# Kernel optimization log

Measured on AMD Instinct MI355X. Metric: run time of the kernel, lower is better.

Reference implementation:

```python
import jax, jax.numpy as jnp
import numpy as np

B, S, E, H = 2, 2048, 1024, 16
D = E // H  # head_dim = 64


def setup_inputs() -> dict:
    key = jax.random.key(0)
    k1, k2, k3 = jax.random.split(key, 3)
    scale_in = 1.0 / np.sqrt(E)
    return {
        "x": jax.random.normal(k1, (B, S, E), dtype=jnp.float32),
        "W_attn": jax.random.normal(k2, (E, 3 * E), dtype=jnp.float32) * scale_in,
        "b_attn": jnp.zeros((3 * E,), dtype=jnp.float32),
        "W_proj": jax.random.normal(k3, (E, E), dtype=jnp.float32) * scale_in,
        "b_proj": jnp.zeros((E,), dtype=jnp.float32),
    }


def reference(x, W_attn, b_attn, W_proj, b_proj):
    # c_attn: fused QKV projection  [B,S,E] -> [B,S,3E]
    qkv = x @ W_attn + b_attn
    q, k, v = jnp.split(qkv, 3, axis=-1)
    # split heads -> [B,S,H,D]
    q = q.reshape(B, S, H, D)
    k = k.reshape(B, S, H, D)
    v = v.reshape(B, S, H, D)
    # scaled dot-product attention (no causal mask in the source module)
    scores = jnp.einsum("bqhd,bkhd->bhqk", q, k) / jnp.sqrt(jnp.float32(D))
    attn = jax.nn.softmax(scores, axis=-1)  # attn_dropout is identity in eval
    y = jnp.einsum("bhqk,bkhd->bqhd", attn, v).reshape(B, S, E)
    # c_proj; resid_dropout is identity in eval
    return y @ W_proj + b_proj
```

## Files before the change

### kernel.cpp

```cpp
#include <hip/hip_runtime.h>
#include <stdint.h>

#define NB 2
#define NS 2048
#define NE 1024
#define NH 16
#define ND 64
#define NE3 3072
#define NBS 4096

typedef _Float16 half8 __attribute__((ext_vector_type(8)));
typedef __fp16 fp16x2 __attribute__((ext_vector_type(2)));
typedef float f32x4 __attribute__((ext_vector_type(4)));
typedef float f32x16 __attribute__((ext_vector_type(16)));
typedef unsigned int u32;

__device__ __forceinline__ void gload16(const void* g, void* l) {
  __builtin_amdgcn_global_load_lds(
      (__attribute__((address_space(1))) void*)const_cast<void*>(g),
      (__attribute__((address_space(3))) void*)l, 16, 0, 0);
}

__global__ void k_cvt16(const float* __restrict__ src, _Float16* __restrict__ dst, int n8) {
  int i = blockIdx.x * blockDim.x + threadIdx.x;
  if (i >= n8) return;
  const float4* s = (const float4*)src + (size_t)i * 2;
  float4 a = s[0], b = s[1];
  half8 o;
  o[0]=(_Float16)a.x; o[1]=(_Float16)a.y; o[2]=(_Float16)a.z; o[3]=(_Float16)a.w;
  o[4]=(_Float16)b.x; o[5]=(_Float16)b.y; o[6]=(_Float16)b.z; o[7]=(_Float16)b.w;
  *((half8*)dst + i) = o;
}

__global__ void k_cvtT(const float* __restrict__ src, _Float16* __restrict__ dst, int K, int N) {
  __shared__ _Float16 tile[64][72];
  int n0 = blockIdx.x * 64, k0 = blockIdx.y * 64;
  int t = threadIdx.x;
  int kk = t >> 2, nc = (t & 3) << 4;
  const float* sp = src + (size_t)(k0 + kk) * N + n0 + nc;
#pragma unroll
  for (int j = 0; j < 16; j += 4) {
    float4 v = *(const float4*)(sp + j);
    tile[kk][nc + j + 0] = (_Float16)v.x;
    tile[kk][nc + j + 1] = (_Float16)v.y;
    tile[kk][nc + j + 2] = (_Float16)v.z;
    tile[kk][nc + j + 3] = (_Float16)v.w;
  }
  __syncthreads();
  int nn = t >> 2, kc = (t & 3) << 4;
  half8 o0, o1;
#pragma unroll
  for (int j = 0; j < 8; ++j) { o0[j] = tile[kc + j][nn]; o1[j] = tile[kc + 8 + j][nn]; }
  _Float16* op = dst + (size_t)(n0 + nn) * K + k0 + kc;
  *(half8*)op = o0;
  *(half8*)(op + 8) = o1;
}

template <int OUT_HALF>
__global__ __launch_bounds__(256, 2)
void k_gemm(const _Float16* __restrict__ A, const _Float16* __restrict__ Bt,
            const float* __restrict__ bias, void* __restrict__ Cv,
            int M, int N, int K) {
  __shared__ _Float16 As[128 * 32];
  __shared__ _Float16 Bs[128 * 32];
  const int nwg = gridDim.x * gridDim.y;
  const int d = blockIdx.y * gridDim.x + blockIdx.x;
  const int lid = (d & 7) * (nwg >> 3) + (d >> 3);
  const int bx = lid % gridDim.x, by = lid / gridDim.x;
  const int m0 = by * 128, n0 = bx * 128;
  const int t = threadIdx.x, l = t & 63, w = t >> 6;
  const int wr = w >> 1, wc = w & 1;
  const int srow = l >> 2;
  const int sk = (l & 3) << 3;
  f32x4 acc[4][4] = {};
  for (int kt = 0; kt < K; kt += 32) {
    __syncthreads();
#pragma unroll
    for (int i = 0; i < 2; ++i) {
      int rb = (i * 4 + w) * 16;
      gload16(A + (size_t)(m0 + rb + srow) * K + kt + sk, (char*)As + (i * 4 + w) * 1024);
      gload16(Bt + (size_t)(n0 + rb + srow) * K + kt + sk, (char*)Bs + (i * 4 + w) * 1024);
    }
    __syncthreads();
    half8 a[4], b[4];
#pragma unroll
    for (int i = 0; i < 4; ++i)
      a[i] = *(const half8*)(As + (wr * 64 + i * 16 + (l & 15)) * 32 + ((l >> 4) << 3));
#pragma unroll
    for (int j = 0; j < 4; ++j)
      b[j] = *(const half8*)(Bs + (wc * 64 + j * 16 + (l & 15)) * 32 + ((l >> 4) << 3));
#pragma unroll
    for (int i = 0; i < 4; ++i)
#pragma unroll
      for (int j = 0; j < 4; ++j)
        acc[i][j] = __builtin_amdgcn_mfma_f32_16x16x32_f16(a[i], b[j], acc[i][j], 0, 0, 0);
  }
  float bv[4];
#pragma unroll
  for (int j = 0; j < 4; ++j) bv[j] = bias[n0 + wc * 64 + j * 16 + (l & 15)];
#pragma unroll
  for (int i = 0; i < 4; ++i) {
    int row0 = m0 + wr * 64 + i * 16 + ((l >> 4) << 2);
#pragma unroll
    for (int j = 0; j < 4; ++j) {
      int col = n0 + wc * 64 + j * 16 + (l & 15);
#pragma unroll
      for (int r = 0; r < 4; ++r) {
        float v = acc[i][j][r] + bv[j];
        if (OUT_HALF)
          ((_Float16*)Cv)[(size_t)(row0 + r) * N + col] = (_Float16)v;
        else
          ((float*)Cv)[(size_t)(row0 + r) * N + col] = v;
      }
    }
  }
}

__global__ void k_vt(const _Float16* __restrict__ qkv, _Float16* __restrict__ Vt) {
  __shared__ _Float16 tile[64][72];
  int s0 = blockIdx.x * 64;
  int bh = blockIdx.y, b = bh >> 4, h = bh & 15;
  int t = threadIdx.x;
  int ss = t >> 2, dc = (t & 3) << 4;
  const _Float16* sp = qkv + (size_t)(b * NS + s0 + ss) * NE3 + 2 * NE + h * ND + dc;
  half8 v0 = *(const half8*)sp, v1 = *(const half8*)(sp + 8);
#pragma unroll
  for (int j = 0; j < 8; ++j) { tile[ss][dc + j] = v0[j]; tile[ss][dc + 8 + j] = v1[j]; }
  __syncthreads();
  int d = t >> 2, sc = (t & 3) << 4;
  half8 o0, o1;
#pragma unroll
  for (int j = 0; j < 8; ++j) { o0[j] = tile[sc + j][d]; o1[j] = tile[sc + 8 + j][d]; }
  _Float16* op = Vt + (size_t)(bh * ND + d) * NS + s0 + sc;
  *(half8*)op = o0;
  *(half8*)(op + 8) = o1;
}

__global__ __launch_bounds__(256, 2)
void k_attn(const _Float16* __restrict__ qkv, const _Float16* __restrict__ Vt,
            _Float16* __restrict__ Y) {
  __shared__ _Float16 Kb[2][64 * 64];
  __shared__ _Float16 Vb[2][64 * 64];
  const int dly = blockIdx.y * gridDim.x + blockIdx.x;
  const int lid = (dly & 7) * 64 + (dly >> 3);
  const int bh = lid >> 4, qb = lid & 15;
  const int q0 = qb * 128;
  const int b = bh >> 4, h = bh & 15;
  const int t = threadIdx.x, l = t & 63, w = t >> 6;
  const int c = l & 31, hh = l >> 5;
  const float cexp = 0.125f * 1.44269504088896340736f;

  half8 qf[4];
  {
    const _Float16* qp = qkv + (size_t)(b * NS + q0 + w * 32 + c) * NE3 + h * ND + 8 * hh;
    qf[0] = *(const half8*)(qp);
    qf[1] = *(const half8*)(qp + 16);
    qf[2] = *(const half8*)(qp + 32);
    qf[3] = *(const half8*)(qp + 48);
  }

  f32x16 Oa0 = {}, Oa1 = {}, Osum = {};
  half8 ones;
#pragma unroll
  for (int j = 0; j < 8; ++j) ones[j] = (_Float16)1.0f;

  const int row8 = l >> 3;
  const int d0s_base = (l & 7) << 3;

#define STAGE_KV(KT, BUF)                                                            \
  {                                                                                  \
    _Pragma("unroll")                                                                \
    for (int i = 0; i < 2; ++i) {                                                    \
      int ci = w * 2 + i;                                                            \
      int row = ci * 8 + row8;                                                       \
      int d0s = d0s_base ^ ((row & 7) << 3);                                         \
      gload16(qkv + (size_t)(b * NS + (KT) * 64 + row) * NE3 + NE + h * ND + d0s,    \
              (char*)&Kb[BUF][0] + ci * 1024);                                       \
      gload16(Vt + (size_t)(bh * ND + row) * NS + (KT) * 64 + d0s,                   \
              (char*)&Vb[BUF][0] + ci * 1024);                                       \
    }                                                                                \
  }

  STAGE_KV(0, 0);
  __syncthreads();

  for (int kt = 0; kt < NS / 64; ++kt) {
    const int cur = kt & 1;
    if (kt + 1 < NS / 64) STAGE_KV(kt + 1, cur ^ 1);

    f32x16 sa0 = {}, sa1 = {};
#pragma unroll
    for (int tt = 0; tt < 4; ++tt) {
      int chs = ((2 * tt + hh) ^ (c & 7)) << 4;
      half8 kf0 = *(const half8*)((char*)&Kb[cur][0] + c * 128 + chs);
      half8 kf1 = *(const half8*)((char*)&Kb[cur][0] + (32 + c) * 128 + chs);
      sa0 = __builtin_amdgcn_mfma_f32_32x32x16_f16(kf0, qf[tt], sa0, 0, 0, 0);
      sa1 = __builtin_amdgcn_mfma_f32_32x32x16_f16(kf1, qf[tt], sa1, 0, 0, 0);
    }

    u32 D0[4][2], D1[4][2];
#pragma unroll
    for (int s = 0; s < 4; ++s) {
      fp16x2 e0 = __builtin_amdgcn_cvt_pkrtz(__builtin_amdgcn_exp2f(sa0[4 * s + 0] * cexp),
                                             __builtin_amdgcn_exp2f(sa0[4 * s + 1] * cexp));
      fp16x2 e1 = __builtin_amdgcn_cvt_pkrtz(__builtin_amdgcn_exp2f(sa0[4 * s + 2] * cexp),
                                             __builtin_amdgcn_exp2f(sa0[4 * s + 3] * cexp));
      fp16x2 e2 = __builtin_amdgcn_cvt_pkrtz(__builtin_amdgcn_exp2f(sa1[4 * s + 0] * cexp),
                                             __builtin_amdgcn_exp2f(sa1[4 * s + 1] * cexp));
      fp16x2 e3 = __builtin_amdgcn_cvt_pkrtz(__builtin_amdgcn_exp2f(sa1[4 * s + 2] * cexp),
                                             __builtin_amdgcn_exp2f(sa1[4 * s + 3] * cexp));
      D0[s][0] = __builtin_bit_cast(u32, e0);
      D0[s][1] = __builtin_bit_cast(u32, e1);
      D1[s][0] = __builtin_bit_cast(u32, e2);
      D1[s][1] = __builtin_bit_cast(u32, e3);
    }

#define PVSTEP(KK, DARR)                                                              \
    {                                                                                 \
      u32 pb0 = DARR[2 * ((KK) & 1)][0], pa0 = DARR[2 * ((KK) & 1) + 1][0];           \
      u32 pb1 = DARR[2 * ((KK) & 1)][1], pa1 = DARR[2 * ((KK) & 1) + 1][1];           \
      u32 sent0 = hh ? pb0 : pa0;                                                     \
      u32 sent1 = hh ? pb1 : pa1;                                                     \
      u32 recv0 = __shfl_xor(sent0, 32);                                              \
      u32 recv1 = __shfl_xor(sent1, 32);                                              \
      union { u32 d[4]; half8 h; } pfu;                                               \
      pfu.d[0] = hh ? recv0 : pb0;                                                    \
      pfu.d[1] = hh ? recv1 : pb1;                                                    \
      pfu.d[2] = hh ? pa0 : recv0;                                                    \
      pfu.d[3] = hh ? pa1 : recv1;                                                    \
      int chv = ((2 * (KK) + hh) ^ (c & 7)) << 4;                                     \
      half8 vf0 = *(const half8*)((char*)&Vb[cur][0] + c * 128 + chv);                \
      half8 vf1 = *(const half8*)((char*)&Vb[cur][0] + (32 + c) * 128 + chv);         \
      Oa0 = __builtin_amdgcn_mfma_f32_32x32x16_f16(pfu.h, vf0, Oa0, 0, 0, 0);         \
      Oa1 = __builtin_amdgcn_mfma_f32_32x32x16_f16(pfu.h, vf1, Oa1, 0, 0, 0);         \
      Osum = __builtin_amdgcn_mfma_f32_32x32x16_f16(pfu.h, ones, Osum, 0, 0, 0);      \
    }
    PVSTEP(0, D0)
    PVSTEP(1, D0)
    PVSTEP(2, D1)
    PVSTEP(3, D1)
#undef PVSTEP

    __syncthreads();
  }

#pragma unroll
  for (int i = 0; i < 16; ++i) {
    int ql = (i & 3) + 8 * (i >> 2) + 4 * hh;
    float inv = 1.0f / Osum[i];
    size_t base = (size_t)(b * NS + q0 + w * 32 + ql) * NE + h * ND + c;
    Y[base] = (_Float16)(Oa0[i] * inv);
    Y[base + 32] = (_Float16)(Oa1[i] * inv);
  }
}

extern "C" void kernel_launch(void* const* d_in, const int* in_sizes, int n_in,
                              void* d_out, int out_size, void* d_ws, size_t ws_size,
                              hipStream_t stream) {
  (void)in_sizes; (void)n_in; (void)out_size; (void)ws_size;
  const float* x      = (const float*)d_in[0];
  const float* W_attn = (const float*)d_in[1];
  const float* b_attn = (const float*)d_in[2];
  const float* W_proj = (const float*)d_in[3];
  const float* b_proj = (const float*)d_in[4];
  char* ws = (char*)d_ws;
  const size_t MB = 1024 * 1024;
  _Float16* qkvb = (_Float16*)(ws);
  _Float16* WaT  = (_Float16*)(ws + 24 * MB);
  _Float16* WpT  = (_Float16*)(ws + 30 * MB);
  _Float16* xb   = (_Float16*)(ws + 32 * MB);
  _Float16* Vt   = (_Float16*)(ws + 40 * MB);
  _Float16* yb   = (_Float16*)(ws + 32 * MB);

  k_cvt16<<<dim3(2048), dim3(256), 0, stream>>>(x, xb, NBS * NE / 8);
  k_cvtT<<<dim3(48, 16), dim3(256), 0, stream>>>(W_attn, WaT, NE, NE3);
  k_cvtT<<<dim3(16, 16), dim3(256), 0, stream>>>(W_proj, WpT, NE, NE);
  k_gemm<1><<<dim3(NE3 / 128, NBS / 128), dim3(256), 0, stream>>>(xb, WaT, b_attn, (void*)qkvb, NBS, NE3, NE);
  k_vt<<<dim3(NS / 64, NB * NH), dim3(256), 0, stream>>>(qkvb, Vt);
  k_attn<<<dim3(NS / 128, NB * NH), dim3(256), 0, stream>>>(qkvb, Vt, yb);
  k_gemm<0><<<dim3(NE / 128, NBS / 128), dim3(256), 0, stream>>>(yb, WpT, b_proj, d_out, NBS, NE, NE);
}
```

Before: 135.6 us.

## Software-pipeline QK of next tile with PV and fold softmax scale into Q

The attention loop is restructured so the QK^T MFMAs for the next key tile are issued between the exp stage and the PV MFMAs of the current tile. K and V staging are split and staggered so K runs one tile further ahead than V. The loop is unrolled by two with ping-pong score registers. Separately, the softmax scale times log2(e) is folded into the Q columns in the QKV GEMM epilogue, which removes a multiply per score element. The cost is higher register pressure, a more complex buffer-reuse schedule, and Q rounded to fp16 after scaling.

```diff
diff --git a/kernel.cpp b/kernel.cpp
--- a/kernel.cpp
+++ b/kernel.cpp
@@ -8,6 +8,7 @@
 #define ND 64
 #define NE3 3072
 #define NBS 4096
+#define NT 32
 
 typedef _Float16 half8 __attribute__((ext_vector_type(8)));
 typedef __fp16 fp16x2 __attribute__((ext_vector_type(2)));
@@ -107,6 +108,7 @@
 #pragma unroll
       for (int r = 0; r < 4; ++r) {
         float v = acc[i][j][r] + bv[j];
+        if (OUT_HALF && col < NE) v *= 0.18033688011112042f;
         if (OUT_HALF)
           ((_Float16*)Cv)[(size_t)(row0 + r) * N + col] = (_Float16)v;
         else
@@ -148,7 +150,6 @@
   const int b = bh >> 4, h = bh & 15;
   const int t = threadIdx.x, l = t & 63, w = t >> 6;
   const int c = l & 31, hh = l >> 5;
-  const float cexp = 0.125f * 1.44269504088896340736f;
 
   half8 qf[4];
   {
@@ -160,6 +161,7 @@
   }
 
   f32x16 Oa0 = {}, Oa1 = {}, Osum = {};
+  f32x16 saE0, saE1, saO0, saO1;
   half8 ones;
 #pragma unroll
   for (int j = 0; j < 8; ++j) ones[j] = (_Float16)1.0f;
@@ -167,7 +169,7 @@
   const int row8 = l >> 3;
   const int d0s_base = (l & 7) << 3;
 
-#define STAGE_KV(KT, BUF)                                                            \
+#define STAGE_K(KT, BUF)                                                             \
   {                                                                                  \
     _Pragma("unroll")                                                                \
     for (int i = 0; i < 2; ++i) {                                                    \
@@ -176,46 +178,34 @@
       int d0s = d0s_base ^ ((row & 7) << 3);                                         \
       gload16(qkv + (size_t)(b * NS + (KT) * 64 + row) * NE3 + NE + h * ND + d0s,    \
               (char*)&Kb[BUF][0] + ci * 1024);                                       \
+    }                                                                                \
+  }
+#define STAGE_V(KT, BUF)                                                             \
+  {                                                                                  \
+    _Pragma("unroll")                                                                \
+    for (int i = 0; i < 2; ++i) {                                                    \
+      int ci = w * 2 + i;                                                            \
+      int row = ci * 8 + row8;                                                       \
+      int d0s = d0s_base ^ ((row & 7) << 3);                                         \
       gload16(Vt + (size_t)(bh * ND + row) * NS + (KT) * 64 + d0s,                   \
               (char*)&Vb[BUF][0] + ci * 1024);                                       \
     }                                                                                \
   }
 
-  STAGE_KV(0, 0);
-  __syncthreads();
-
-  for (int kt = 0; kt < NS / 64; ++kt) {
-    const int cur = kt & 1;
-    if (kt + 1 < NS / 64) STAGE_KV(kt + 1, cur ^ 1);
-
-    f32x16 sa0 = {}, sa1 = {};
-#pragma unroll
-    for (int tt = 0; tt < 4; ++tt) {
-      int chs = ((2 * tt + hh) ^ (c & 7)) << 4;
-      half8 kf0 = *(const half8*)((char*)&Kb[cur][0] + c * 128 + chs);
-      half8 kf1 = *(const half8*)((char*)&Kb[cur][0] + (32 + c) * 128 + chs);
-      sa0 = __builtin_amdgcn_mfma_f32_32x32x16_f16(kf0, qf[tt], sa0, 0, 0, 0);
-      sa1 = __builtin_amdgcn_mfma_f32_32x32x16_f16(kf1, qf[tt], sa1, 0, 0, 0);
-    }
-
-    u32 D0[4][2], D1[4][2];
-#pragma unroll
-    for (int s = 0; s < 4; ++s) {
-      fp16x2 e0 = __builtin_amdgcn_cvt_pkrtz(__builtin_amdgcn_exp2f(sa0[4 * s + 0] * cexp),
-                                             __builtin_amdgcn_exp2f(sa0[4 * s + 1] * cexp));
-      fp16x2 e1 = __builtin_amdgcn_cvt_pkrtz(__builtin_amdgcn_exp2f(sa0[4 * s + 2] * cexp),
-                                             __builtin_amdgcn_exp2f(sa0[4 * s + 3] * cexp));
-      fp16x2 e2 = __builtin_amdgcn_cvt_pkrtz(__builtin_amdgcn_exp2f(sa1[4 * s + 0] * cexp),
-                                             __builtin_amdgcn_exp2f(sa1[4 * s + 1] * cexp));
-      fp16x2 e3 = __builtin_amdgcn_cvt_pkrtz(__builtin_amdgcn_exp2f(sa1[4 * s + 2] * cexp),
-                                             __builtin_amdgcn_exp2f(sa1[4 * s + 3] * cexp));
-      D0[s][0] = __builtin_bit_cast(u32, e0);
-      D0[s][1] = __builtin_bit_cast(u32, e1);
-      D1[s][0] = __builtin_bit_cast(u32, e2);
-      D1[s][1] = __builtin_bit_cast(u32, e3);
-    }
-
-#define PVSTEP(KK, DARR)                                                              \
+#define QK_TILE(BUF, SA0, SA1)                                                       \
+  {                                                                                  \
+    SA0 = (f32x16){}; SA1 = (f32x16){};                                              \
+    _Pragma("unroll")                                                                \
+    for (int tt = 0; tt < 4; ++tt) {                                                 \
+      int chs = ((2 * tt + hh) ^ (c & 7)) << 4;                                      \
+      half8 kf0 = *(const half8*)((char*)&Kb[BUF][0] + c * 128 + chs);               \
+      half8 kf1 = *(const half8*)((char*)&Kb[BUF][0] + (32 + c) * 128 + chs);        \
+      SA0 = __builtin_amdgcn_mfma_f32_32x32x16_f16(kf0, qf[tt], SA0, 0, 0, 0);       \
+      SA1 = __builtin_amdgcn_mfma_f32_32x32x16_f16(kf1, qf[tt], SA1, 0, 0, 0);       \
+    }                                                                                \
+  }
+
+#define PVSTEP(KK, DARR, CUR)                                                         \
     {                                                                                 \
       u32 pb0 = DARR[2 * ((KK) & 1)][0], pa0 = DARR[2 * ((KK) & 1) + 1][0];           \
       u32 pb1 = DARR[2 * ((KK) & 1)][1], pa1 = DARR[2 * ((KK) & 1) + 1][1];           \
@@ -229,20 +219,59 @@
       pfu.d[2] = hh ? pa0 : recv0;                                                    \
       pfu.d[3] = hh ? pa1 : recv1;                                                    \
       int chv = ((2 * (KK) + hh) ^ (c & 7)) << 4;                                     \
-      half8 vf0 = *(const half8*)((char*)&Vb[cur][0] + c * 128 + chv);                \
-      half8 vf1 = *(const half8*)((char*)&Vb[cur][0] + (32 + c) * 128 + chv);         \
+      half8 vf0 = *(const half8*)((char*)&Vb[CUR][0] + c * 128 + chv);                \
+      half8 vf1 = *(const half8*)((char*)&Vb[CUR][0] + (32 + c) * 128 + chv);         \
       Oa0 = __builtin_amdgcn_mfma_f32_32x32x16_f16(pfu.h, vf0, Oa0, 0, 0, 0);         \
       Oa1 = __builtin_amdgcn_mfma_f32_32x32x16_f16(pfu.h, vf1, Oa1, 0, 0, 0);         \
       Osum = __builtin_amdgcn_mfma_f32_32x32x16_f16(pfu.h, ones, Osum, 0, 0, 0);      \
     }
-    PVSTEP(0, D0)
-    PVSTEP(1, D0)
-    PVSTEP(2, D1)
-    PVSTEP(3, D1)
+
+#define TILE_BODY(T, CUR, SAC0, SAC1, SAN0, SAN1)                                     \
+  {                                                                                   \
+    u32 D0[4][2], D1[4][2];                                                           \
+    _Pragma("unroll")                                                                 \
+    for (int s = 0; s < 4; ++s) {                                                     \
+      fp16x2 e0 = __builtin_amdgcn_cvt_pkrtz(__builtin_amdgcn_exp2f(SAC0[4 * s + 0]), \
+                                             __builtin_amdgcn_exp2f(SAC0[4 * s + 1]));\
+      fp16x2 e1 = __builtin_amdgcn_cvt_pkrtz(__builtin_amdgcn_exp2f(SAC0[4 * s + 2]), \
+                                             __builtin_amdgcn_exp2f(SAC0[4 * s + 3]));\
+      fp16x2 e2 = __builtin_amdgcn_cvt_pkrtz(__builtin_amdgcn_exp2f(SAC1[4 * s + 0]), \
+                                             __builtin_amdgcn_exp2f(SAC1[4 * s + 1]));\
+      fp16x2 e3 = __builtin_amdgcn_cvt_pkrtz(__builtin_amdgcn_exp2f(SAC1[4 * s + 2]), \
+                                             __builtin_amdgcn_exp2f(SAC1[4 * s + 3]));\
+      D0[s][0] = __builtin_bit_cast(u32, e0);                                         \
+      D0[s][1] = __builtin_bit_cast(u32, e1);                                         \
+      D1[s][0] = __builtin_bit_cast(u32, e2);                                         \
+      D1[s][1] = __builtin_bit_cast(u32, e3);                                         \
+    }                                                                                 \
+    if ((T) + 1 < NT) QK_TILE((CUR) ^ 1, SAN0, SAN1);                                 \
+    PVSTEP(0, D0, CUR)                                                                \
+    PVSTEP(1, D0, CUR)                                                                \
+    PVSTEP(2, D1, CUR)                                                                \
+    PVSTEP(3, D1, CUR)                                                                \
+    __syncthreads();                                                                  \
+    if ((T) + 2 < NT) STAGE_V((T) + 2, CUR);                                          \
+    if ((T) + 3 < NT) STAGE_K((T) + 3, (CUR) ^ 1);                                    \
+  }
+
+  STAGE_K(0, 0);
+  STAGE_V(0, 0);
+  STAGE_K(1, 1);
+  __syncthreads();
+  QK_TILE(0, saE0, saE1);
+  __syncthreads();
+  STAGE_V(1, 1);
+  STAGE_K(2, 0);
+
+  for (int kt = 0; kt < NT; kt += 2) {
+    TILE_BODY(kt, 0, saE0, saE1, saO0, saO1);
+    TILE_BODY(kt + 1, 1, saO0, saO1, saE0, saE1);
+  }
+#undef TILE_BODY
 #undef PVSTEP
-
-    __syncthreads();
-  }
+#undef QK_TILE
+#undef STAGE_K
+#undef STAGE_V
 
 #pragma unroll
   for (int i = 0; i < 16; ++i) {
```

Result: faster. 129.4 us (-4.6%).
